# Kernel tuning notes

Hardware: AMD Instinct MI355X
Metric: run time of the kernel (lower is better)

Reference implementation:

```python
import jax, jax.numpy as jnp
import numpy as np

N = 50000      # nodes
E = 800000     # edges
INIT = 256     # input feature dim
HID = 64       # per-head hidden dim
EMB = 128      # output embed dim
H = 8          # heads
ALPHA = 0.2    # leaky-relu slope
EPS = 1e-16    # guard for isolated nodes


def setup_inputs() -> dict:
    key = jax.random.key(0)
    ks = jax.random.split(key, 6)
    x = jax.random.normal(ks[0], (N, INIT), dtype=jnp.float32)
    edge_index = jax.random.randint(ks[1], (2, E), 0, N, dtype=jnp.int32)
    # xavier-ish scaling keeps exp(-leakyrelu(.)) in a sane range
    W1 = jax.random.normal(ks[2], (H, INIT, HID), dtype=jnp.float32) / np.sqrt(INIT).astype(np.float32)
    a1 = jax.random.normal(ks[3], (H, 2 * HID), dtype=jnp.float32) / np.sqrt(2 * HID).astype(np.float32)
    Wo = jax.random.normal(ks[4], (H * HID, EMB), dtype=jnp.float32) / np.sqrt(H * HID).astype(np.float32)
    ao = jax.random.normal(ks[5], (2 * EMB,), dtype=jnp.float32) / np.sqrt(2 * EMB).astype(np.float32)
    return {"x": x, "edge_index": edge_index, "W1": W1, "a1": a1, "Wo": Wo, "ao": ao}


def _sp_att_head(x, W, a, src, dst):
    """One sparse GAT head (pyGAT SpGraphAttentionLayer math)."""
    h = x @ W                                              # [N, F']
    eh = jnp.concatenate([h[src], h[dst]], axis=1)          # [E, 2F']
    ee = jnp.exp(-jax.nn.leaky_relu(eh @ a, ALPHA))         # [E]
    denom = jax.ops.segment_sum(ee, src, num_segments=N) + EPS          # [N]
    num = jax.ops.segment_sum(ee[:, None] * h[dst], src, num_segments=N)  # [N, F']
    h_prime = num / denom[:, None]
    att = ee / denom[src]
    return h_prime, att


def reference(x, edge_index, W1, a1, Wo, ao, args=0):
    src, dst = edge_index[0], edge_index[1]
    # first (and only) multi-head layer, concat=True -> elu per head, concat on feature dim
    heads = [jax.nn.elu(_sp_att_head(x, W1[i], a1[i], src, dst)[0]) for i in range(H)]
    x1 = jnp.concatenate(heads, axis=1)                     # [N, H*HID]
    # output attention layer, concat=False; top-level applies elu
    h_prime, att_out = _sp_att_head(x1, Wo, ao, src, dst)
    return jax.nn.elu(h_prime), edge_index, att_out
```

## Files before the change

kernel.cpp:

```cpp
#include <hip/hip_runtime.h>
#include <hip/hip_bf16.h>
#include <cstddef>

#define NN    50000
#define NE    800000
#define FIN   256
#define HID   64
#define NH    8
#define F1    512
#define EMB   128
#define ALPHA 0.2f
#define EPSF  1e-16f
#define NBLK  ((NN + 255) / 256)

#if defined(__has_builtin)
# if __has_builtin(__builtin_amdgcn_cvt_scalef32_pk_f32_fp4) && __has_builtin(__builtin_amdgcn_cvt_scalef32_pk_fp4_f32)
#  define HAVE_FP4 1
# else
#  define HAVE_FP4 0
# endif
#else
# define HAVE_FP4 0
#endif

typedef __hip_bfloat16 bf16;
typedef __attribute__((ext_vector_type(8))) short short8;
typedef __attribute__((ext_vector_type(4))) float f32x4;
typedef __attribute__((ext_vector_type(2))) float f32x2;

#if HAVE_FP4
typedef uint2 pay_t;
#define PAYB1 (F1 / 2)
#define PAYB2 (EMB / 2)
#define SINV1 2.0f
#define SINV2 4.0f
#define PSC1  0.5f
#define PSC2  0.25f
#else
typedef uint4 pay_t;
#define PAYB1 F1
#define PAYB2 EMB
#define SINV1 1.0f
#define SINV2 1.0f
#define PSC1  1.0f
#define PSC2  1.0f
#endif

__device__ __forceinline__ float eluf(float x){ return x > 0.f ? x : expm1f(x); }
__device__ __forceinline__ float lrelu_neg_exp(float s){
    float lr = s > 0.f ? s : ALPHA * s;
    return __expf(-lr);
}
__device__ __forceinline__ float b2f(unsigned u){ return __uint_as_float(u << 16); }

__device__ __forceinline__ void fma16(float* acc, pay_t q, float e){
#if HAVE_FP4
#define D4(w, s, o) { f32x2 p = __builtin_amdgcn_cvt_scalef32_pk_f32_fp4((w), 1.0f, (s)); \
                      acc[(o)] += e * p[0]; acc[(o) + 1] += e * p[1]; }
    D4(q.x, 0, 0)  D4(q.x, 1, 2)  D4(q.x, 2, 4)  D4(q.x, 3, 6)
    D4(q.y, 0, 8)  D4(q.y, 1, 10) D4(q.y, 2, 12) D4(q.y, 3, 14)
#undef D4
#else
#define D8(w, o) { f32x2 p0 = __builtin_amdgcn_cvt_pk_f32_fp8((w), false); \
                   f32x2 p1 = __builtin_amdgcn_cvt_pk_f32_fp8((w), true); \
                   acc[(o)] += e * p0[0]; acc[(o)+1] += e * p0[1]; \
                   acc[(o)+2] += e * p1[0]; acc[(o)+3] += e * p1[1]; }
    D8(q.x, 0) D8(q.y, 4) D8(q.z, 8) D8(q.w, 12)
#undef D8
#endif
}

__device__ __forceinline__ unsigned bpack(float a, float b){
    unsigned ua = __float_as_uint(a), ub = __float_as_uint(b);
    ua = (ua + 0x7fffu + ((ua >> 16) & 1)) >> 16;
    ub = (ub + 0x7fffu + ((ub >> 16) & 1)) >> 16;
    return (ua & 0xffffu) | (ub << 16);
}

__global__ void k_cvt_x(const float* __restrict__ x, bf16* __restrict__ xb){
    int i = blockIdx.x * 256 + threadIdx.x;
    if (i >= NN * FIN / 8) return;
    const float4* xp = (const float4*)(x + (size_t)i * 8);
    float4 v0 = xp[0], v1 = xp[1];
    uint4 o;
    o.x = bpack(v0.x, v0.y); o.y = bpack(v0.z, v0.w);
    o.z = bpack(v1.x, v1.y); o.w = bpack(v1.z, v1.w);
    *(uint4*)(xb + (size_t)i * 8) = o;
}

__global__ void k_tw1(const float* __restrict__ W1, bf16* __restrict__ Bt1){
    int i = blockIdx.x * 256 + threadIdx.x;
    if (i >= F1 * FIN) return;
    int n = i >> 8, k = i & 255;
    Bt1[i] = __float2bfloat16(W1[(size_t)(n >> 6) * FIN * HID + (size_t)k * HID + (n & 63)]);
}

__global__ void k_tw2(const float* __restrict__ Wo, bf16* __restrict__ WoT){
    int i = blockIdx.x * 256 + threadIdx.x;
    if (i >= EMB * F1) return;
    int n = i >> 9, k = i & 511;
    WoT[i] = __float2bfloat16(Wo[(size_t)k * EMB + n]);
}

__global__ void k_q4(const unsigned char* __restrict__ in, unsigned* __restrict__ out,
                     int n8, float sinv){
    int i = blockIdx.x * 256 + threadIdx.x;
    if (i >= n8) return;
    uint2 v = *(const uint2*)(in + (size_t)i * 8);
#if HAVE_FP4
    f32x2 a = __builtin_amdgcn_cvt_pk_f32_fp8(v.x, false);
    f32x2 b = __builtin_amdgcn_cvt_pk_f32_fp8(v.x, true);
    f32x2 c = __builtin_amdgcn_cvt_pk_f32_fp8(v.y, false);
    f32x2 d = __builtin_amdgcn_cvt_pk_f32_fp8(v.y, true);
    unsigned r = 0;
    r = __builtin_amdgcn_cvt_scalef32_pk_fp4_f32(r, a[0] * sinv, a[1] * sinv, 1.0f, 0);
    r = __builtin_amdgcn_cvt_scalef32_pk_fp4_f32(r, b[0] * sinv, b[1] * sinv, 1.0f, 1);
    r = __builtin_amdgcn_cvt_scalef32_pk_fp4_f32(r, c[0] * sinv, c[1] * sinv, 1.0f, 2);
    r = __builtin_amdgcn_cvt_scalef32_pk_fp4_f32(r, d[0] * sinv, d[1] * sinv, 1.0f, 3);
    out[i] = r;
#else
    (void)sinv;
    *(uint2*)((unsigned char*)out + (size_t)i * 8) = v;
#endif
}

__global__ void k_zero(int* p, int n){
    int i = blockIdx.x * 256 + threadIdx.x;
    if (i < n) p[i] = 0;
}

__global__ void k_count(const int* __restrict__ src, int* __restrict__ cnt){
    int e = blockIdx.x * 256 + threadIdx.x;
    if (e < NE) atomicAdd(&cnt[src[e]], 1);
}

__global__ __launch_bounds__(256) void k_bsum(const int* __restrict__ cnt, int* __restrict__ bsum){
    const int b = blockIdx.x, t = threadIdx.x, idx = b * 256 + t;
    int v = (idx < NN) ? cnt[idx] : 0;
#pragma unroll
    for (int o = 1; o < 64; o <<= 1) v += __shfl_xor(v, o);
    __shared__ int ws[4];
    if ((t & 63) == 0) ws[t >> 6] = v;
    __syncthreads();
    if (t == 0) bsum[b] = ws[0] + ws[1] + ws[2] + ws[3];
}

__global__ __launch_bounds__(256) void k_scanb(const int* __restrict__ bsum,
                                               int* __restrict__ boff,
                                               int* __restrict__ rp){
    const int t = threadIdx.x;
    __shared__ int s[256];
    const int v = (t < NBLK) ? bsum[t] : 0;
    s[t] = v;
    __syncthreads();
    for (int o = 1; o < 256; o <<= 1){
        int u = (t >= o) ? s[t - o] : 0;
        __syncthreads();
        s[t] += u;
        __syncthreads();
    }
    if (t < NBLK) boff[t] = s[t] - v;
    if (t == 255) rp[NN] = s[255];
}

__global__ __launch_bounds__(256) void k_rp(const int* __restrict__ cnt,
                                            const int* __restrict__ boff,
                                            int* __restrict__ rp){
    const int b = blockIdx.x, t = threadIdx.x, idx = b * 256 + t;
    const int v = (idx < NN) ? cnt[idx] : 0;
    __shared__ int s[256];
    s[t] = v;
    __syncthreads();
    for (int o = 1; o < 256; o <<= 1){
        int u = (t >= o) ? s[t - o] : 0;
        __syncthreads();
        s[t] += u;
        __syncthreads();
    }
    if (idx < NN) rp[idx] = boff[b] + s[t] - v;
}

__global__ void k_scatter(const int* __restrict__ src, const int* __restrict__ dst,
                          const int* __restrict__ rp, int* __restrict__ cur,
                          int* __restrict__ sdst){
    int e = blockIdx.x * 256 + threadIdx.x;
    if (e < NE){
        int s = src[e];
        int p = atomicAdd(&cur[s], 1);
        sdst[rp[s] + p] = dst[e];
    }
}

template<int K>
__global__ __launch_bounds__(256) void k_mgemm(const bf16* __restrict__ A,
                                               const bf16* __restrict__ B,
                                               unsigned char* __restrict__ C,
                                               int N){
    constexpr int LDT = 40;
    __shared__ __align__(16) bf16 As[128 * LDT];
    __shared__ __align__(16) bf16 Bs[128 * LDT];
    const int t = threadIdx.x;
    const int lane = t & 63, wid = t >> 6;
    const int m0 = blockIdx.x * 128, n0 = blockIdx.y * 128;
    const int r0 = t >> 2, u0 = t & 3;
    const int r1 = r0 + 64;
    const int rb = (wid & 1) * 64, cb = (wid >> 1) * 64;
    const int fr = lane & 15, fk = (lane >> 4) * 8;

    f32x4 acc[4][4];
#pragma unroll
    for (int i = 0; i < 4; i++)
#pragma unroll
        for (int j = 0; j < 4; j++) acc[i][j] = (f32x4)(0.f);

    for (int k0 = 0; k0 < K; k0 += 32){
        const int ga0 = m0 + r0, ga1 = m0 + r1;
        uint4 av0 = (ga0 < NN) ? *(const uint4*)(A + (size_t)ga0 * K + k0 + u0 * 8)
                               : make_uint4(0, 0, 0, 0);
        uint4 av1 = (ga1 < NN) ? *(const uint4*)(A + (size_t)ga1 * K + k0 + u0 * 8)
                               : make_uint4(0, 0, 0, 0);
        uint4 bv0 = *(const uint4*)(B + (size_t)(n0 + r0) * K + k0 + u0 * 8);
        uint4 bv1 = *(const uint4*)(B + (size_t)(n0 + r1) * K + k0 + u0 * 8);
        __syncthreads();
        *(uint4*)(As + r0 * LDT + u0 * 8) = av0;
        *(uint4*)(As + r1 * LDT + u0 * 8) = av1;
        *(uint4*)(Bs + r0 * LDT + u0 * 8) = bv0;
        *(uint4*)(Bs + r1 * LDT + u0 * 8) = bv1;
        __syncthreads();
        short8 af[4], bf_[4];
#pragma unroll
        for (int i = 0; i < 4; i++){
            af[i]  = *(const short8*)(As + (rb + i * 16 + fr) * LDT + fk);
            bf_[i] = *(const short8*)(Bs + (cb + i * 16 + fr) * LDT + fk);
        }
#pragma unroll
        for (int i = 0; i < 4; i++)
#pragma unroll
            for (int j = 0; j < 4; j++)
                acc[i][j] = __builtin_amdgcn_mfma_f32_16x16x32_bf16(af[i], bf_[j], acc[i][j], 0, 0, 0);
    }
    const int crow = m0 + rb + (lane >> 4) * 4;
    const int ccol = n0 + cb + (lane & 15);
#pragma unroll
    for (int i = 0; i < 4; i++)
#pragma unroll
        for (int j = 0; j < 4; j++)
#pragma unroll
            for (int v = 0; v < 4; v++){
                int row = crow + i * 16 + v;
                if (row < NN){
                    float val = acc[i][j][v];
                    unsigned r = __builtin_amdgcn_cvt_pk_fp8_f32(val, val, 0u, false);
                    C[(size_t)row * N + ccol + j * 16] = (unsigned char)(r & 0xffu);
                }
            }
}

__global__ void k_s1(const unsigned char* __restrict__ h1q, const float* __restrict__ a1,
                     float* __restrict__ s11, float* __restrict__ s12){
    int idx = blockIdx.x * 256 + threadIdx.x;
    if (idx >= NN * NH) return;
    int n = idx >> 3, h = idx & 7;
    const uint4* hp = (const uint4*)(h1q + (size_t)n * F1 + h * HID);
    const float* a  = a1 + (size_t)h * 2 * HID;
    float d1 = 0.f, d2 = 0.f;
#pragma unroll
    for (int u = 0; u < 4; u++){
        uint4 q = hp[u];
        int j = u * 16;
#define S2(w, o) { f32x2 p0 = __builtin_amdgcn_cvt_pk_f32_fp8((w), false); \
                   f32x2 p1 = __builtin_amdgcn_cvt_pk_f32_fp8((w), true); \
                   d1 += p0[0]*a[(o)] + p0[1]*a[(o)+1] + p1[0]*a[(o)+2] + p1[1]*a[(o)+3]; \
                   d2 += p0[0]*a[HID+(o)] + p0[1]*a[HID+(o)+1] + p1[0]*a[HID+(o)+2] + p1[1]*a[HID+(o)+3]; }
        S2(q.x, j) S2(q.y, j + 4) S2(q.z, j + 8) S2(q.w, j + 12)
#undef S2
    }
    s11[idx] = d1;
    s12[idx] = d2;
}

__global__ __launch_bounds__(256) void k_agg1(const unsigned char* __restrict__ hq,
                                              const float* __restrict__ s11,
                                              const float* __restrict__ s12,
                                              const int* __restrict__ rp,
                                              const int* __restrict__ sdst,
                                              bf16* __restrict__ x1){
    const int t = threadIdx.x, lane = t & 63, w = t >> 6;
    const int n = blockIdx.x * 4 + w;
    const int ha = lane & 7;
    const int l32 = lane & 31;
    const int half = lane >> 5;
    const int hf = l32 >> 2;
    const float s1a = s11[n * NH + ha];
    float acc[16];
#pragma unroll
    for (int i = 0; i < 16; i++) acc[i] = 0.f;
    float dedp = 0.f;
    const int start = rp[n], end = rp[n + 1];
    const unsigned char* __restrict__ hl = hq + (size_t)l32 * (PAYB1 / 32);
    for (int c0 = start; c0 < end; c0 += 64){
        const int m = min(64, end - c0);
        int dreg = (lane < m) ? sdst[c0 + lane] : 0;
        for (int sc = 0; sc < m; sc += 8){
            int el = sc + (lane >> 3);
            int de = __shfl(dreg, el & 63);
            float ev = (el < m) ? lrelu_neg_exp(s1a + s12[de * NH + ha]) : 0.f;
            dedp += ev;
#pragma unroll 4
            for (int p = 0; p < 4 && sc + 2 * p < m; p++){
                float ej = __shfl(ev, ((2 * p + half) << 3) + hf);
                int   dj = __shfl(dreg, (sc + 2 * p + half) & 63);
                pay_t q = *(const pay_t*)(hl + (size_t)dj * PAYB1);
                fma16(acc, q, ej);
            }
        }
    }
    dedp += __shfl_xor(dedp, 8);
    dedp += __shfl_xor(dedp, 16);
    dedp += __shfl_xor(dedp, 32);
#pragma unroll
    for (int i = 0; i < 16; i++) acc[i] += __shfl_xor(acc[i], 32);
    float ded = __shfl(dedp, hf);
    const float inv = PSC1 / (ded + EPSF);
    if (half == 0){
        float o[16];
#pragma unroll
        for (int i = 0; i < 16; i++) o[i] = eluf(acc[i] * inv);
        uint4 ov0, ov1;
        ov0.x = bpack(o[0], o[1]);   ov0.y = bpack(o[2], o[3]);
        ov0.z = bpack(o[4], o[5]);   ov0.w = bpack(o[6], o[7]);
        ov1.x = bpack(o[8], o[9]);   ov1.y = bpack(o[10], o[11]);
        ov1.z = bpack(o[12], o[13]); ov1.w = bpack(o[14], o[15]);
        bf16* xp = x1 + (size_t)n * F1 + l32 * 16;
        *(uint4*)xp = ov0;
        *(uint4*)(xp + 8) = ov1;
    }
}

__global__ void k_s2(const unsigned char* __restrict__ h2q, const float* __restrict__ ao,
                     float* __restrict__ s21, float* __restrict__ s22){
    int n = blockIdx.x * 256 + threadIdx.x;
    if (n >= NN) return;
    const uint4* hp = (const uint4*)(h2q + (size_t)n * EMB);
    float d1 = 0.f, d2 = 0.f;
#pragma unroll
    for (int u = 0; u < 8; u++){
        uint4 q = hp[u];
        int j = u * 16;
#define S2(w, o) { f32x2 p0 = __builtin_amdgcn_cvt_pk_f32_fp8((w), false); \
                   f32x2 p1 = __builtin_amdgcn_cvt_pk_f32_fp8((w), true); \
                   d1 += p0[0]*ao[(o)] + p0[1]*ao[(o)+1] + p1[0]*ao[(o)+2] + p1[1]*ao[(o)+3]; \
                   d2 += p0[0]*ao[EMB+(o)] + p0[1]*ao[EMB+(o)+1] + p1[0]*ao[EMB+(o)+2] + p1[1]*ao[EMB+(o)+3]; }
        S2(q.x, j) S2(q.y, j + 4) S2(q.z, j + 8) S2(q.w, j + 12)
#undef S2
    }
    s21[n] = d1;
    s22[n] = d2;
}

__global__ __launch_bounds__(256) void k_agg2(const unsigned char* __restrict__ hq,
                                              const float* __restrict__ s21,
                                              const float* __restrict__ s22,
                                              const int* __restrict__ rp,
                                              const int* __restrict__ sdst,
                                              float* __restrict__ den2,
                                              float* __restrict__ out0){
    const int t = threadIdx.x, lane = t & 63, w = t >> 6;
    const int n = blockIdx.x * 4 + w;
    const int slot = lane >> 3;
    const int fpos = lane & 7;
    const float s1v = s21[n];
    float acc[16];
#pragma unroll
    for (int i = 0; i < 16; i++) acc[i] = 0.f;
    float dedp = 0.f;
    const int start = rp[n], end = rp[n + 1];
    const unsigned char* __restrict__ hl = hq + (size_t)fpos * (PAYB2 / 8);
    for (int c0 = start; c0 < end; c0 += 64){
        const int m = min(64, end - c0);
        int dreg = (lane < m) ? sdst[c0 + lane] : 0;
        float ev = (lane < m) ? lrelu_neg_exp(s1v + s22[dreg]) : 0.f;
        dedp += ev;
        for (int j = 0; j < m; j += 8){
            int ei = j + slot;
            if (ei < m){
                int   d = __shfl(dreg, ei);
                float e = __shfl(ev, ei);
                pay_t q = *(const pay_t*)(hl + (size_t)d * PAYB2);
                fma16(acc, q, e);
            }
        }
    }
#pragma unroll
    for (int o = 1; o <= 32; o <<= 1) dedp += __shfl_xor(dedp, o);
#pragma unroll
    for (int o = 8; o <= 32; o <<= 1)
#pragma unroll
        for (int i = 0; i < 16; i++) acc[i] += __shfl_xor(acc[i], o);
    const float den = dedp + EPSF;
    if (slot == 0){
        const float inv = PSC2 / den;
        float* op = out0 + (size_t)n * EMB + fpos * 16;
#pragma unroll
        for (int u = 0; u < 4; u++){
            float4 ov;
            ov.x = eluf(acc[u * 4 + 0] * inv);
            ov.y = eluf(acc[u * 4 + 1] * inv);
            ov.z = eluf(acc[u * 4 + 2] * inv);
            ov.w = eluf(acc[u * 4 + 3] * inv);
            *(float4*)(op + u * 4) = ov;
        }
        if (lane == 0) den2[n] = den;
    }
}

__global__ void k_att_edge(const int* __restrict__ ei,
                           const float* __restrict__ s21, const float* __restrict__ s22,
                           const float* __restrict__ den2,
                           float* __restrict__ outE, float* __restrict__ outA){
    int i = blockIdx.x * 256 + threadIdx.x;
    if (i < 2 * NE) outE[i] = (float)ei[i];
    if (i < NE){
        int s = ei[i], d = ei[NE + i];
        float ee = lrelu_neg_exp(s21[s] + s22[d]);
        outA[i] = ee / den2[s];
    }
}

extern "C" void kernel_launch(void* const* d_in, const int* in_sizes, int n_in,
                              void* d_out, int out_size, void* d_ws, size_t ws_size,
                              hipStream_t stream){
    const float* x  = (const float*)d_in[0];
    const int*   ei = (const int*)d_in[1];
    const float* W1 = (const float*)d_in[2];
    const float* a1 = (const float*)d_in[3];
    const float* Wo = (const float*)d_in[4];
    const float* ao = (const float*)d_in[5];
    float* out = (float*)d_out;
    const int* src = ei;
    const int* dst = ei + NE;

    char* w = (char*)d_ws;
    auto alloc = [&](size_t bytes) -> char* {
        char* p = w;
        w += (bytes + 255) & ~(size_t)255;
        return p;
    };
    bf16*  xb   = (bf16*) alloc((size_t)NN * FIN * 2);
    bf16*  x1   = (bf16*) alloc((size_t)NN * F1 * 2);
    unsigned char* h1q = (unsigned char*)alloc((size_t)NN * F1);
    unsigned char* h2q = (unsigned char*)alloc((size_t)NN * EMB);
    bf16*  Bt1  = (bf16*) alloc((size_t)F1 * FIN * 2);
    bf16*  WoT  = (bf16*) alloc((size_t)EMB * F1 * 2);
    float* s11  = (float*)alloc((size_t)NN * NH * 4);
    float* s12  = (float*)alloc((size_t)NN * NH * 4);
    float* s21  = (float*)alloc((size_t)NN * 4);
    float* s22  = (float*)alloc((size_t)NN * 4);
    float* den2 = (float*)alloc((size_t)NN * 4);
    int*   cnt2 = (int*)  alloc((size_t)2 * NN * 4);
    int*   rp   = (int*)  alloc((size_t)(NN + 1) * 4);
    int*   sdst = (int*)  alloc((size_t)NE * 4);
    int*   bsum = (int*)  alloc((size_t)NBLK * 4);
    int*   boff = (int*)  alloc((size_t)NBLK * 4);
    int*   cnt = cnt2;
    int*   cur = cnt2 + NN;
    unsigned char* h1pay = (unsigned char*)xb;
    unsigned char* h2pay = (unsigned char*)x1;

    k_cvt_x<<<(NN * FIN / 8 + 255) / 256, 256, 0, stream>>>(x, xb);
    k_tw1  <<<(F1 * FIN + 255) / 256,     256, 0, stream>>>(W1, Bt1);
    k_tw2  <<<(EMB * F1 + 255) / 256,     256, 0, stream>>>(Wo, WoT);

    k_zero   <<<(2 * NN + 255) / 256, 256, 0, stream>>>(cnt2, 2 * NN);
    k_count  <<<(NE + 255) / 256,     256, 0, stream>>>(src, cnt);
    k_bsum   <<<NBLK,                 256, 0, stream>>>(cnt, bsum);
    k_scanb  <<<1,                    256, 0, stream>>>(bsum, boff, rp);
    k_rp     <<<NBLK,                 256, 0, stream>>>(cnt, boff, rp);
    k_scatter<<<(NE + 255) / 256,     256, 0, stream>>>(src, dst, rp, cur, sdst);

    k_mgemm<FIN><<<dim3((NN + 127) / 128, F1 / 128), 256, 0, stream>>>(xb, Bt1, h1q, F1);
    k_q4  <<<(NN * F1 / 8 + 255) / 256, 256, 0, stream>>>(h1q, (unsigned*)h1pay, NN * F1 / 8, SINV1);
    k_s1  <<<(NN * NH + 255) / 256, 256, 0, stream>>>(h1q, a1, s11, s12);
    k_agg1<<<NN / 4, 256, 0, stream>>>(h1pay, s11, s12, rp, sdst, x1);

    k_mgemm<F1><<<dim3((NN + 127) / 128, EMB / 128), 256, 0, stream>>>(x1, WoT, h2q, EMB);
    k_q4  <<<(NN * EMB / 8 + 255) / 256, 256, 0, stream>>>(h2q, (unsigned*)h2pay, NN * EMB / 8, SINV2);
    k_s2  <<<(NN + 255) / 256, 256, 0, stream>>>(h2q, ao, s21, s22);
    k_agg2<<<NN / 4, 256, 0, stream>>>(h2pay, s21, s22, rp, sdst, den2, out);

    k_att_edge<<<(2 * NE + 255) / 256, 256, 0, stream>>>(ei, s21, s22, den2,
                                                         out + (size_t)NN * EMB,
                                                         out + (size_t)NN * EMB + 2 * NE);
}
```

Measured before the change: 331.1 us.

## Fuse input bf16 conversion into GEMM1 and FP4 quantization into score kernel

Result: faster. 321.3 us (-2.9%).

```diff
diff --git a/kernel.cpp b/kernel.cpp
--- a/kernel.cpp
+++ b/kernel.cpp
@@ -53,20 +53,26 @@
 }
 __device__ __forceinline__ float b2f(unsigned u){ return __uint_as_float(u << 16); }
 
-__device__ __forceinline__ void fma16(float* acc, pay_t q, float e){
+__device__ __forceinline__ void fma16pk(f32x2* acc, pay_t q, float e){
+    f32x2 e2; e2[0] = e; e2[1] = e;
 #if HAVE_FP4
-#define D4(w, s, o) { f32x2 p = __builtin_amdgcn_cvt_scalef32_pk_f32_fp4((w), 1.0f, (s)); \
-                      acc[(o)] += e * p[0]; acc[(o) + 1] += e * p[1]; }
-    D4(q.x, 0, 0)  D4(q.x, 1, 2)  D4(q.x, 2, 4)  D4(q.x, 3, 6)
-    D4(q.y, 0, 8)  D4(q.y, 1, 10) D4(q.y, 2, 12) D4(q.y, 3, 14)
-#undef D4
+    acc[0] += __builtin_amdgcn_cvt_scalef32_pk_f32_fp4(q.x, 1.0f, 0) * e2;
+    acc[1] += __builtin_amdgcn_cvt_scalef32_pk_f32_fp4(q.x, 1.0f, 1) * e2;
+    acc[2] += __builtin_amdgcn_cvt_scalef32_pk_f32_fp4(q.x, 1.0f, 2) * e2;
+    acc[3] += __builtin_amdgcn_cvt_scalef32_pk_f32_fp4(q.x, 1.0f, 3) * e2;
+    acc[4] += __builtin_amdgcn_cvt_scalef32_pk_f32_fp4(q.y, 1.0f, 0) * e2;
+    acc[5] += __builtin_amdgcn_cvt_scalef32_pk_f32_fp4(q.y, 1.0f, 1) * e2;
+    acc[6] += __builtin_amdgcn_cvt_scalef32_pk_f32_fp4(q.y, 1.0f, 2) * e2;
+    acc[7] += __builtin_amdgcn_cvt_scalef32_pk_f32_fp4(q.y, 1.0f, 3) * e2;
 #else
-#define D8(w, o) { f32x2 p0 = __builtin_amdgcn_cvt_pk_f32_fp8((w), false); \
-                   f32x2 p1 = __builtin_amdgcn_cvt_pk_f32_fp8((w), true); \
-                   acc[(o)] += e * p0[0]; acc[(o)+1] += e * p0[1]; \
-                   acc[(o)+2] += e * p1[0]; acc[(o)+3] += e * p1[1]; }
-    D8(q.x, 0) D8(q.y, 4) D8(q.z, 8) D8(q.w, 12)
-#undef D8
+    acc[0] += __builtin_amdgcn_cvt_pk_f32_fp8(q.x, false) * e2;
+    acc[1] += __builtin_amdgcn_cvt_pk_f32_fp8(q.x, true)  * e2;
+    acc[2] += __builtin_amdgcn_cvt_pk_f32_fp8(q.y, false) * e2;
+    acc[3] += __builtin_amdgcn_cvt_pk_f32_fp8(q.y, true)  * e2;
+    acc[4] += __builtin_amdgcn_cvt_pk_f32_fp8(q.z, false) * e2;
+    acc[5] += __builtin_amdgcn_cvt_pk_f32_fp8(q.z, true)  * e2;
+    acc[6] += __builtin_amdgcn_cvt_pk_f32_fp8(q.w, false) * e2;
+    acc[7] += __builtin_amdgcn_cvt_pk_f32_fp8(q.w, true)  * e2;
 #endif
 }
 
@@ -75,17 +81,6 @@
     ua = (ua + 0x7fffu + ((ua >> 16) & 1)) >> 16;
     ub = (ub + 0x7fffu + ((ub >> 16) & 1)) >> 16;
     return (ua & 0xffffu) | (ub << 16);
-}
-
-__global__ void k_cvt_x(const float* __restrict__ x, bf16* __restrict__ xb){
-    int i = blockIdx.x * 256 + threadIdx.x;
-    if (i >= NN * FIN / 8) return;
-    const float4* xp = (const float4*)(x + (size_t)i * 8);
-    float4 v0 = xp[0], v1 = xp[1];
-    uint4 o;
-    o.x = bpack(v0.x, v0.y); o.y = bpack(v0.z, v0.w);
-    o.z = bpack(v1.x, v1.y); o.w = bpack(v1.z, v1.w);
-    *(uint4*)(xb + (size_t)i * 8) = o;
 }
 
 __global__ void k_tw1(const float* __restrict__ W1, bf16* __restrict__ Bt1){
@@ -191,6 +186,80 @@
     }
 }
 
+__global__ __launch_bounds__(256) void k_gemm1f(const float* __restrict__ A,
+                                                const bf16* __restrict__ B,
+                                                unsigned char* __restrict__ C){
+    constexpr int K = FIN, N = F1;
+    constexpr int LDT = 40;
+    __shared__ __align__(16) bf16 As[128 * LDT];
+    __shared__ __align__(16) bf16 Bs[128 * LDT];
+    const int t = threadIdx.x;
+    const int lane = t & 63, wid = t >> 6;
+    const int m0 = blockIdx.x * 128, n0 = blockIdx.y * 128;
+    const int r0 = t >> 2, u0 = t & 3;
+    const int r1 = r0 + 64;
+    const int rb = (wid & 1) * 64, cb = (wid >> 1) * 64;
+    const int fr = lane & 15, fk = (lane >> 4) * 8;
+
+    f32x4 acc[4][4];
+#pragma unroll
+    for (int i = 0; i < 4; i++)
+#pragma unroll
+        for (int j = 0; j < 4; j++) acc[i][j] = (f32x4)(0.f);
+
+    for (int k0 = 0; k0 < K; k0 += 32){
+        const int ga0 = m0 + r0, ga1 = m0 + r1;
+        float4 a0a = make_float4(0,0,0,0), a0b = a0a, a1a = a0a, a1b = a0a;
+        if (ga0 < NN){
+            const float* p = A + (size_t)ga0 * K + k0 + u0 * 8;
+            a0a = *(const float4*)p; a0b = *(const float4*)(p + 4);
+        }
+        if (ga1 < NN){
+            const float* p = A + (size_t)ga1 * K + k0 + u0 * 8;
+            a1a = *(const float4*)p; a1b = *(const float4*)(p + 4);
+        }
+        uint4 av0, av1;
+        av0.x = bpack(a0a.x, a0a.y); av0.y = bpack(a0a.z, a0a.w);
+        av0.z = bpack(a0b.x, a0b.y); av0.w = bpack(a0b.z, a0b.w);
+        av1.x = bpack(a1a.x, a1a.y); av1.y = bpack(a1a.z, a1a.w);
+        av1.z = bpack(a1b.x, a1b.y); av1.w = bpack(a1b.z, a1b.w);
+        uint4 bv0 = *(const uint4*)(B + (size_t)(n0 + r0) * K + k0 + u0 * 8);
+        uint4 bv1 = *(const uint4*)(B + (size_t)(n0 + r1) * K + k0 + u0 * 8);
+        __syncthreads();
+        *(uint4*)(As + r0 * LDT + u0 * 8) = av0;
+        *(uint4*)(As + r1 * LDT + u0 * 8) = av1;
+        *(uint4*)(Bs + r0 * LDT + u0 * 8) = bv0;
+        *(uint4*)(Bs + r1 * LDT + u0 * 8) = bv1;
+        __syncthreads();
+        short8 af[4], bf_[4];
+#pragma unroll
+        for (int i = 0; i < 4; i++){
+            af[i]  = *(const short8*)(As + (rb + i * 16 + fr) * LDT + fk);
+            bf_[i] = *(const short8*)(Bs + (cb + i * 16 + fr) * LDT + fk);
+        }
+#pragma unroll
+        for (int i = 0; i < 4; i++)
+#pragma unroll
+            for (int j = 0; j < 4; j++)
+                acc[i][j] = __builtin_amdgcn_mfma_f32_16x16x32_bf16(af[i], bf_[j], acc[i][j], 0, 0, 0);
+    }
+    const int crow = m0 + rb + (lane >> 4) * 4;
+    const int ccol = n0 + cb + (lane & 15);
+#pragma unroll
+    for (int i = 0; i < 4; i++)
+#pragma unroll
+        for (int j = 0; j < 4; j++)
+#pragma unroll
+            for (int v = 0; v < 4; v++){
+                int row = crow + i * 16 + v;
+                if (row < NN){
+                    float val = acc[i][j][v];
+                    unsigned r = __builtin_amdgcn_cvt_pk_fp8_f32(val, val, 0u, false);
+                    C[(size_t)row * N + ccol + j * 16] = (unsigned char)(r & 0xffu);
+                }
+            }
+}
+
 template<int K>
 __global__ __launch_bounds__(256) void k_mgemm(const bf16* __restrict__ A,
                                                const bf16* __restrict__ B,
@@ -256,27 +325,70 @@
             }
 }
 
-__global__ void k_s1(const unsigned char* __restrict__ h1q, const float* __restrict__ a1,
-                     float* __restrict__ s11, float* __restrict__ s12){
+__global__ void k_s1q(const unsigned char* __restrict__ h1q, const float* __restrict__ a1,
+                      float* __restrict__ s11, float* __restrict__ s12,
+                      unsigned char* __restrict__ pay){
     int idx = blockIdx.x * 256 + threadIdx.x;
     if (idx >= NN * NH) return;
     int n = idx >> 3, h = idx & 7;
     const uint4* hp = (const uint4*)(h1q + (size_t)n * F1 + h * HID);
     const float* a  = a1 + (size_t)h * 2 * HID;
     float d1 = 0.f, d2 = 0.f;
+    float f[64];
 #pragma unroll
     for (int u = 0; u < 4; u++){
         uint4 q = hp[u];
         int j = u * 16;
-#define S2(w, o) { f32x2 p0 = __builtin_amdgcn_cvt_pk_f32_fp8((w), false); \
-                   f32x2 p1 = __builtin_amdgcn_cvt_pk_f32_fp8((w), true); \
-                   d1 += p0[0]*a[(o)] + p0[1]*a[(o)+1] + p1[0]*a[(o)+2] + p1[1]*a[(o)+3]; \
-                   d2 += p0[0]*a[HID+(o)] + p0[1]*a[HID+(o)+1] + p1[0]*a[HID+(o)+2] + p1[1]*a[HID+(o)+3]; }
-        S2(q.x, j) S2(q.y, j + 4) S2(q.z, j + 8) S2(q.w, j + 12)
-#undef S2
+        f32x2 p;
+        p = __builtin_amdgcn_cvt_pk_f32_fp8(q.x, false); f[j+0]=p[0];  f[j+1]=p[1];
+        p = __builtin_amdgcn_cvt_pk_f32_fp8(q.x, true);  f[j+2]=p[0];  f[j+3]=p[1];
+        p = __builtin_amdgcn_cvt_pk_f32_fp8(q.y, false); f[j+4]=p[0];  f[j+5]=p[1];
+        p = __builtin_amdgcn_cvt_pk_f32_fp8(q.y, true);  f[j+6]=p[0];  f[j+7]=p[1];
+        p = __builtin_amdgcn_cvt_pk_f32_fp8(q.z, false); f[j+8]=p[0];  f[j+9]=p[1];
+        p = __builtin_amdgcn_cvt_pk_f32_fp8(q.z, true);  f[j+10]=p[0]; f[j+11]=p[1];
+        p = __builtin_amdgcn_cvt_pk_f32_fp8(q.w, false); f[j+12]=p[0]; f[j+13]=p[1];
+        p = __builtin_amdgcn_cvt_pk_f32_fp8(q.w, true);  f[j+14]=p[0]; f[j+15]=p[1];
+    }
+#pragma unroll
+    for (int j = 0; j < 64; j++){
+        d1 += f[j] * a[j];
+        d2 += f[j] * a[HID + j];
     }
     s11[idx] = d1;
     s12[idx] = d2;
+#if HAVE_FP4
+    unsigned r[4];
+#pragma unroll
+    for (int u = 0; u < 4; u++){
+        unsigned rr = 0;
+        int j = u * 16;
+        rr = __builtin_amdgcn_cvt_scalef32_pk_fp4_f32(rr, f[j+0]*SINV1,  f[j+1]*SINV1,  1.0f, 0);
+        rr = __builtin_amdgcn_cvt_scalef32_pk_fp4_f32(rr, f[j+2]*SINV1,  f[j+3]*SINV1,  1.0f, 1);
+        rr = __builtin_amdgcn_cvt_scalef32_pk_fp4_f32(rr, f[j+4]*SINV1,  f[j+5]*SINV1,  1.0f, 2);
+        rr = __builtin_amdgcn_cvt_scalef32_pk_fp4_f32(rr, f[j+6]*SINV1,  f[j+7]*SINV1,  1.0f, 3);
+        r[u] = rr;
+        (void)j;
+    }
+    unsigned w8[8];
+#pragma unroll
+    for (int u = 0; u < 8; u++){
+        unsigned rr = 0;
+        int j = u * 8;
+        rr = __builtin_amdgcn_cvt_scalef32_pk_fp4_f32(rr, f[j+0]*SINV1, f[j+1]*SINV1, 1.0f, 0);
+        rr = __builtin_amdgcn_cvt_scalef32_pk_fp4_f32(rr, f[j+2]*SINV1, f[j+3]*SINV1, 1.0f, 1);
+        rr = __builtin_amdgcn_cvt_scalef32_pk_fp4_f32(rr, f[j+4]*SINV1, f[j+5]*SINV1, 1.0f, 2);
+        rr = __builtin_amdgcn_cvt_scalef32_pk_fp4_f32(rr, f[j+6]*SINV1, f[j+7]*SINV1, 1.0f, 3);
+        w8[u] = rr;
+    }
+    uint4* op = (uint4*)(pay + (size_t)n * PAYB1 + h * (HID / 2));
+    uint4 o0, o1;
+    o0.x = w8[0]; o0.y = w8[1]; o0.z = w8[2]; o0.w = w8[3];
+    o1.x = w8[4]; o1.y = w8[5]; o1.z = w8[6]; o1.w = w8[7];
+    op[0] = o0; op[1] = o1;
+#else
+    uint4* op = (uint4*)(pay + (size_t)n * PAYB1 + h * HID);
+    op[0] = hp[0]; op[1] = hp[1]; op[2] = hp[2]; op[3] = hp[3];
+#endif
 }
 
 __global__ __launch_bounds__(256) void k_agg1(const unsigned char* __restrict__ hq,
@@ -291,10 +403,11 @@
     const int l32 = lane & 31;
     const int half = lane >> 5;
     const int hf = l32 >> 2;
+    const int es = lane >> 3;
     const float s1a = s11[n * NH + ha];
-    float acc[16];
-#pragma unroll
-    for (int i = 0; i < 16; i++) acc[i] = 0.f;
+    f32x2 acc[8];
+#pragma unroll
+    for (int i = 0; i < 8; i++){ acc[i][0] = 0.f; acc[i][1] = 0.f; }
     float dedp = 0.f;
     const int start = rp[n], end = rp[n + 1];
     const unsigned char* __restrict__ hl = hq + (size_t)l32 * (PAYB1 / 32);
@@ -302,16 +415,16 @@
         const int m = min(64, end - c0);
         int dreg = (lane < m) ? sdst[c0 + lane] : 0;
         for (int sc = 0; sc < m; sc += 8){
-            int el = sc + (lane >> 3);
-            int de = __shfl(dreg, el & 63);
-            float ev = (el < m) ? lrelu_neg_exp(s1a + s12[de * NH + ha]) : 0.f;
+            const int el = sc + es;
+            const int de = __shfl(dreg, el);
+            const float ev = (el < m) ? lrelu_neg_exp(s1a + s12[de * NH + ha]) : 0.f;
             dedp += ev;
-#pragma unroll 4
-            for (int p = 0; p < 4 && sc + 2 * p < m; p++){
-                float ej = __shfl(ev, ((2 * p + half) << 3) + hf);
-                int   dj = __shfl(dreg, (sc + 2 * p + half) & 63);
+#pragma unroll
+            for (int p = 0; p < 4; p++){
+                const float ej = __shfl(ev, ((2 * p + half) << 3) + hf);
+                const int   dj = __shfl(dreg, sc + 2 * p + half);
                 pay_t q = *(const pay_t*)(hl + (size_t)dj * PAYB1);
-                fma16(acc, q, ej);
+                fma16pk(acc, q, ej);
             }
         }
     }
@@ -319,13 +432,19 @@
     dedp += __shfl_xor(dedp, 16);
     dedp += __shfl_xor(dedp, 32);
 #pragma unroll
-    for (int i = 0; i < 16; i++) acc[i] += __shfl_xor(acc[i], 32);
+    for (int i = 0; i < 8; i++){
+        acc[i][0] += __shfl_xor(acc[i][0], 32);
+        acc[i][1] += __shfl_xor(acc[i][1], 32);
+    }
     float ded = __shfl(dedp, hf);
     const float inv = PSC1 / (ded + EPSF);
     if (half == 0){
         float o[16];
 #pragma unroll
-        for (int i = 0; i < 16; i++) o[i] = eluf(acc[i] * inv);
+        for (int i = 0; i < 8; i++){
+            o[2 * i]     = eluf(acc[i][0] * inv);
+            o[2 * i + 1] = eluf(acc[i][1] * inv);
+        }
         uint4 ov0, ov1;
         ov0.x = bpack(o[0], o[1]);   ov0.y = bpack(o[2], o[3]);
         ov0.z = bpack(o[4], o[5]);   ov0.w = bpack(o[6], o[7]);
@@ -370,9 +489,9 @@
     const int slot = lane >> 3;
     const int fpos = lane & 7;
     const float s1v = s21[n];
-    float acc[16];
-#pragma unroll
-    for (int i = 0; i < 16; i++) acc[i] = 0.f;
+    f32x2 acc[8];
+#pragma unroll
+    for (int i = 0; i < 8; i++){ acc[i][0] = 0.f; acc[i][1] = 0.f; }
     float dedp = 0.f;
     const int start = rp[n], end = rp[n + 1];
     const unsigned char* __restrict__ hl = hq + (size_t)fpos * (PAYB2 / 8);
@@ -382,13 +501,11 @@
         float ev = (lane < m) ? lrelu_neg_exp(s1v + s22[dreg]) : 0.f;
         dedp += ev;
         for (int j = 0; j < m; j += 8){
-            int ei = j + slot;
-            if (ei < m){
-                int   d = __shfl(dreg, ei);
-                float e = __shfl(ev, ei);
-                pay_t q = *(const pay_t*)(hl + (size_t)d * PAYB2);
-                fma16(acc, q, e);
-            }
+            const int ei = j + slot;
+            const float e = __shfl(ev, ei);
+            const int   d = __shfl(dreg, ei);
+            pay_t q = *(const pay_t*)(hl + (size_t)d * PAYB2);
+            fma16pk(acc, q, e);
         }
     }
 #pragma unroll
@@ -396,7 +513,10 @@
 #pragma unroll
     for (int o = 8; o <= 32; o <<= 1)
 #pragma unroll
-        for (int i = 0; i < 16; i++) acc[i] += __shfl_xor(acc[i], o);
+        for (int i = 0; i < 8; i++){
+            acc[i][0] += __shfl_xor(acc[i][0], o);
+            acc[i][1] += __shfl_xor(acc[i][1], o);
+        }
     const float den = dedp + EPSF;
     if (slot == 0){
         const float inv = PSC2 / den;
@@ -404,10 +524,10 @@
 #pragma unroll
         for (int u = 0; u < 4; u++){
             float4 ov;
-            ov.x = eluf(acc[u * 4 + 0] * inv);
-            ov.y = eluf(acc[u * 4 + 1] * inv);
-            ov.z = eluf(acc[u * 4 + 2] * inv);
-            ov.w = eluf(acc[u * 4 + 3] * inv);
+            ov.x = eluf(acc[2 * u][0] * inv);
+            ov.y = eluf(acc[2 * u][1] * inv);
+            ov.z = eluf(acc[2 * u + 1][0] * inv);
+            ov.w = eluf(acc[2 * u + 1][1] * inv);
             *(float4*)(op + u * 4) = ov;
         }
         if (lane == 0) den2[n] = den;
@@ -446,7 +566,7 @@
         w += (bytes + 255) & ~(size_t)255;
         return p;
     };
-    bf16*  xb   = (bf16*) alloc((size_t)NN * FIN * 2);
+    unsigned char* h1pay = (unsigned char*)alloc((size_t)NN * F1);
     bf16*  x1   = (bf16*) alloc((size_t)NN * F1 * 2);
     unsigned char* h1q = (unsigned char*)alloc((size_t)NN * F1);
     unsigned char* h2q = (unsigned char*)alloc((size_t)NN * EMB);
@@ -464,12 +584,10 @@
     int*   boff = (int*)  alloc((size_t)NBLK * 4);
     int*   cnt = cnt2;
     int*   cur = cnt2 + NN;
-    unsigned char* h1pay = (unsigned char*)xb;
     unsigned char* h2pay = (unsigned char*)x1;
 
-    k_cvt_x<<<(NN * FIN / 8 + 255) / 256, 256, 0, stream>>>(x, xb);
-    k_tw1  <<<(F1 * FIN + 255) / 256,     256, 0, stream>>>(W1, Bt1);
-    k_tw2  <<<(EMB * F1 + 255) / 256,     256, 0, stream>>>(Wo, WoT);
+    k_tw1<<<(F1 * FIN + 255) / 256, 256, 0, stream>>>(W1, Bt1);
+    k_tw2<<<(EMB * F1 + 255) / 256, 256, 0, stream>>>(Wo, WoT);
 
     k_zero   <<<(2 * NN + 255) / 256, 256, 0, stream>>>(cnt2, 2 * NN);
     k_count  <<<(NE + 255) / 256,     256, 0, stream>>>(src, cnt);
@@ -478,9 +596,8 @@
     k_rp     <<<NBLK,                 256, 0, stream>>>(cnt, boff, rp);
     k_scatter<<<(NE + 255) / 256,     256, 0, stream>>>(src, dst, rp, cur, sdst);
 
-    k_mgemm<FIN><<<dim3((NN + 127) / 128, F1 / 128), 256, 0, stream>>>(xb, Bt1, h1q, F1);
-    k_q4  <<<(NN * F1 / 8 + 255) / 256, 256, 0, stream>>>(h1q, (unsigned*)h1pay, NN * F1 / 8, SINV1);
-    k_s1  <<<(NN * NH + 255) / 256, 256, 0, stream>>>(h1q, a1, s11, s12);
+    k_gemm1f<<<dim3((NN + 127) / 128, F1 / 128), 256, 0, stream>>>(x, Bt1, h1q);
+    k_s1q <<<(NN * NH + 255) / 256, 256, 0, stream>>>(h1q, a1, s11, s12, h1pay);
     k_agg1<<<NN / 4, 256, 0, stream>>>(h1pay, s11, s12, rp, sdst, x1);
 
     k_mgemm<F1><<<dim3((NN + 127) / 128, EMB / 128), 256, 0, stream>>>(x1, WoT, h2q, EMB);
```
